# Optimization experiments

Hardware: AMD Instinct MI355X
Metric: run time of the kernel (lower is better)

Reference implementation:

```python
import jax, jax.numpy as jnp
import numpy as np

N_NODES = 100000
N_EDGES = 1600000
N_FEAT = 128
N_HID = 128
N_CLASS = 10
N_GRAPHS = 512
BN_EPS = 1e-5


def setup_inputs() -> dict:
    key = jax.random.key(0)
    ks = jax.random.split(key, 12)
    x = jax.random.normal(ks[0], (N_NODES, N_FEAT), dtype=jnp.float32)
    edge_index = jax.random.randint(ks[1], (2, N_EDGES), 0, N_NODES, dtype=jnp.int32)
    batch = jnp.sort(jax.random.randint(ks[2], (N_NODES,), 0, N_GRAPHS, dtype=jnp.int32))
    s1 = 1.0 / np.sqrt(N_FEAT)
    s2 = 1.0 / np.sqrt(N_HID)
    W1 = jax.random.uniform(ks[3], (N_FEAT, N_HID), jnp.float32, -s1, s1)
    b1 = jax.random.uniform(ks[4], (N_HID,), jnp.float32, -s1, s1)
    gamma = jnp.ones((N_HID,), jnp.float32)
    beta = jnp.zeros((N_HID,), jnp.float32)
    W2 = jax.random.uniform(ks[5], (N_HID, N_HID), jnp.float32, -s2, s2)
    b2 = jax.random.uniform(ks[6], (N_HID,), jnp.float32, -s2, s2)
    clsW = jax.random.uniform(ks[7], (N_HID, N_CLASS), jnp.float32, -s2, s2)
    clsb = jax.random.uniform(ks[8], (N_CLASS,), jnp.float32, -s2, s2)
    return {"x": x, "edge_index": edge_index, "batch": batch,
            "W1": W1, "b1": b1, "gamma": gamma, "beta": beta,
            "W2": W2, "b2": b2, "clsW": clsW, "clsb": clsb}


def _gcn_norm(edge_index, n_nodes):
    # add self-loops, compute symmetric normalization D^-1/2 A_hat D^-1/2
    loops = jnp.arange(n_nodes, dtype=edge_index.dtype)
    src = jnp.concatenate([edge_index[0], loops])
    dst = jnp.concatenate([edge_index[1], loops])
    deg = jax.ops.segment_sum(jnp.ones_like(dst, dtype=jnp.float32), dst,
                              num_segments=n_nodes)
    dinv = jnp.where(deg > 0, jax.lax.rsqrt(deg), 0.0)
    norm = dinv[src] * dinv[dst]  # [E + N]
    return src, dst, norm


def _gcn_conv(h, src, dst, norm, W, b, n_nodes):
    h = h @ W                                   # [N, nhid] dense GEMM
    msg = h[src] * norm[:, None]                # gather + scale  [E+N, nhid]
    out = jax.ops.segment_sum(msg, dst, num_segments=n_nodes)  # scatter-add
    return out + b


def reference(x, edge_index, batch, W1, b1, gamma, beta, W2, b2, clsW, clsb):
    n_nodes = x.shape[0]
    src, dst, norm = _gcn_norm(edge_index, n_nodes)
    # layer 1: GCNConv -> BatchNorm(eval, running stats 0/1) -> ReLU -> Dropout(eval=id)
    h = _gcn_conv(x, src, dst, norm, W1, b1, n_nodes)
    h = h * (gamma / jnp.sqrt(1.0 + BN_EPS)) + beta
    h = jax.nn.relu(h)
    # layer 2: GCNConv (output layer, no bn/act)
    h = _gcn_conv(h, src, dst, norm, W2, b2, n_nodes)
    # global mean pool over batch index
    sums = jax.ops.segment_sum(h, batch, num_segments=N_GRAPHS)          # [G, nhid]
    cnts = jax.ops.segment_sum(jnp.ones((n_nodes,), h.dtype), batch,
                               num_segments=N_GRAPHS)
    g = sums / jnp.maximum(cnts, 1.0)[:, None]
    out = jax.nn.log_softmax(g @ clsW + clsb, axis=1)                    # [G, nclass]
    return out, g
```

## Files before the change

kernel.cpp:

```cpp
#include <hip/hip_runtime.h>
#include <hip/hip_bf16.h>

#define N_NODES 100000
#define N_EDGES 1600000
#define N_FEAT 128
#define N_HID 128
#define N_CLASS 10
#define N_GRAPHS 512
#define BN_RSQRT 0.9999950000374997f

#define NRANGE 12500
#define NSUB 512
#define SCAP 640
#define HGROUP 32
#define BPB (NSUB / HGROUP)

#define XT_STRIDE 136
#define YW_STRIDE 36

typedef _Float16 half_t;
typedef __attribute__((ext_vector_type(2))) _Float16 half2v;
typedef __attribute__((ext_vector_type(4))) _Float16 half4v;
typedef __attribute__((ext_vector_type(8))) _Float16 half8v;
typedef __attribute__((ext_vector_type(4))) float floatx4;
typedef __attribute__((ext_vector_type(2))) float floatx2;

__global__ __launch_bounds__(256) void bucket_fused(
    const int* __restrict__ src, const int* __restrict__ dst,
    int* __restrict__ cnt, unsigned long long* __restrict__ bucketed,
    const float* __restrict__ W1, half_t* __restrict__ Wt1,
    const float* __restrict__ W2, half_t* __restrict__ Wt2,
    const int* __restrict__ batch, int* __restrict__ boffs,
    int chunkE, int E, int nnodes)
{
    __shared__ int wcnt[4][8];
    __shared__ int wbase[4][8];
    int blk = blockIdx.x;
    if (blk >= NSUB) {
        int k = blk - NSUB;
        if (k < 128) {
            int i = k * 256 + threadIdx.x;
            const float* W = (i < 16384) ? W1 : W2;
            half_t* Wt = (i < 16384) ? Wt1 : Wt2;
            int j = i & 16383;
            int c = j >> 7, kk = j & 127;
            Wt[(size_t)c * 128 + kk] = (half_t)W[(size_t)kk * 128 + c];
        } else {
            int i = (k - 128) * 256 + threadIdx.x;
            if (i < nnodes) {
                int b = batch[i];
                int prev = (i == 0) ? -1 : batch[i - 1];
                for (int g = prev + 1; g <= b; ++g) boffs[g] = i;
                if (i == nnodes - 1)
                    for (int g = b + 1; g <= N_GRAPHS; ++g) boffs[g] = nnodes;
            }
        }
        return;
    }
    int b = blk;
    int wave = threadIdx.x >> 6;
    int lane = threadIdx.x & 63;
    int e0 = b * chunkE;
    int e1 = e0 + chunkE < E ? e0 + chunkE : E;
    int iters = (chunkE + 255) / 256;

    int mycnt = 0;
    for (int it = 0; it < iters; ++it) {
        int e = e0 + it * 256 + threadIdx.x;
        bool valid = e < e1;
        int d = valid ? dst[e] : 0;
        int rr = (d * 8) / N_NODES;
#pragma unroll
        for (int r = 0; r < 8; ++r) {
            unsigned long long m = __ballot(valid && rr == r);
            if (lane == r) mycnt += __popcll(m);
        }
    }
    if (lane < 8) wcnt[wave][lane] = mycnt;
    __syncthreads();
    if (threadIdx.x < 8) {
        int r = threadIdx.x;
        int s = 0;
#pragma unroll
        for (int w = 0; w < 4; ++w) { wbase[w][r] = s; s += wcnt[w][r]; }
        cnt[r * NSUB + b] = s;
    }
    __syncthreads();

    int myoff = (lane < 8) ? wbase[wave][lane] : 0;
    for (int it = 0; it < iters; ++it) {
        int e = e0 + it * 256 + threadIdx.x;
        bool valid = e < e1;
        int s = valid ? src[e] : 0;
        int d = valid ? dst[e] : 0;
        int rr = (d * 8) / N_NODES;
        unsigned long long pk = ((unsigned long long)(unsigned)d << 32) | (unsigned)s;
#pragma unroll
        for (int r = 0; r < 8; ++r) {
            unsigned long long m = __ballot(valid && rr == r);
            int base_r = __shfl(myoff, r);
            if (valid && rr == r) {
                int pos = base_r + __popcll(m & ((1ull << lane) - 1));
                if (pos < SCAP)
                    bucketed[(size_t)(r * NSUB + b) * SCAP + pos] = pk;
            }
            if (lane == r) myoff += __popcll(m);
        }
    }
}

__global__ __launch_bounds__(256) void hist2(
    const unsigned long long* __restrict__ bucketed, const int* __restrict__ cnt,
    int* __restrict__ partial)
{
    __shared__ int h[NRANGE];
    int r = blockIdx.x & 7, g = blockIdx.x >> 3;
    for (int i = threadIdx.x; i < NRANGE; i += 256) h[i] = 0;
    __syncthreads();
    int rbase = r * NRANGE;
    for (int j = 0; j < BPB; ++j) {
        int b = g * BPB + j;
        int n = cnt[r * NSUB + b];
        if (n > SCAP) n = SCAP;
        const unsigned long long* seg = bucketed + (size_t)(r * NSUB + b) * SCAP;
        for (int i = threadIdx.x; i < n; i += 256)
            atomicAdd(&h[(int)(seg[i] >> 32) - rbase], 1);
    }
    __syncthreads();
    int* slice = partial + (size_t)(r * HGROUP + g) * NRANGE;
    for (int i = threadIdx.x; i < NRANGE; i += 256) slice[i] = h[i];
}

__global__ void deg_reduce(const int* __restrict__ partial, int* __restrict__ deg,
                           float* __restrict__ dinv, int* __restrict__ bsums, int n) {
    __shared__ int sm[256];
    int t = threadIdx.x;
    int i = blockIdx.x * 256 + t;
    int s = 0;
    if (i < n) {
        int rr = i / NRANGE;
        int dl = i - rr * NRANGE;
        const int* p = partial + (size_t)rr * HGROUP * NRANGE + dl;
#pragma unroll 8
        for (int g = 0; g < HGROUP; ++g) s += p[(size_t)g * NRANGE];
        deg[i] = s;
        dinv[i] = rsqrtf((float)s + 1.0f);
    }
    sm[t] = s;
    __syncthreads();
    for (int off = 128; off > 0; off >>= 1) {
        if (t < off) sm[t] += sm[t + off];
        __syncthreads();
    }
    if (t == 0) bsums[blockIdx.x] = sm[0];
}

__global__ void scan_small(int* __restrict__ bsums, int nb) {
    __shared__ int buf[1024];
    int t = threadIdx.x;
    int v = (t < nb) ? bsums[t] : 0;
    buf[t] = v;
    __syncthreads();
    for (int off = 1; off < 1024; off <<= 1) {
        int x = (t >= off) ? buf[t - off] : 0;
        __syncthreads();
        buf[t] += x;
        __syncthreads();
    }
    if (t < nb) bsums[t] = buf[t] - v;
}

__global__ __launch_bounds__(256) void scan_chunkoff(
    const int* __restrict__ in, const int* __restrict__ bsums,
    int* __restrict__ rowptr, int* __restrict__ partial, int n, int total)
{
    __shared__ int s[256];
    int t = threadIdx.x;
    int i = blockIdx.x * 256 + t;
    int v = (i < n) ? in[i] : 0;
    s[t] = v;
    __syncthreads();
    for (int off = 1; off < 256; off <<= 1) {
        int x = (t >= off) ? s[t - off] : 0;
        __syncthreads();
        s[t] += x;
        __syncthreads();
    }
    if (i == 0) rowptr[n] = total;
    if (i < n) {
        int excl = bsums[blockIdx.x] + s[t] - v;
        rowptr[i] = excl;
        int rr = i / NRANGE;
        int dl = i - rr * NRANGE;
        int* p = partial + (size_t)rr * HGROUP * NRANGE + dl;
        int vals[32];
#pragma unroll
        for (int g = 0; g < 32; ++g) vals[g] = p[(size_t)g * NRANGE];
        int running = excl;
#pragma unroll
        for (int g = 0; g < 32; ++g) {
            int tmp = vals[g];
            p[(size_t)g * NRANGE] = running;
            running += tmp;
        }
    }
}

__global__ __launch_bounds__(256) void fill2(
    const unsigned long long* __restrict__ bucketed, const int* __restrict__ cnt,
    const int* __restrict__ partial, int* __restrict__ col)
{
    __shared__ int off[NRANGE];
    int r = blockIdx.x & 7, g = blockIdx.x >> 3;
    const int* slice = partial + (size_t)(r * HGROUP + g) * NRANGE;
    for (int i = threadIdx.x; i < NRANGE; i += 256) off[i] = slice[i];
    __syncthreads();
    int rbase = r * NRANGE;
    for (int j = 0; j < BPB; ++j) {
        int b = g * BPB + j;
        int n = cnt[r * NSUB + b];
        if (n > SCAP) n = SCAP;
        const unsigned long long* seg = bucketed + (size_t)(r * NSUB + b) * SCAP;
        for (int i = threadIdx.x; i < n; i += 256) {
            unsigned long long pk = seg[i];
            int pos = atomicAdd(&off[(int)(pk >> 32) - rbase], 1);
            col[pos] = (int)((unsigned)(pk & 0xffffffffu) << 7);
        }
    }
}

__global__ __launch_bounds__(256, 2) void gemm1_mfma(
    const float* __restrict__ X, const half_t* __restrict__ Wt,
    const float* __restrict__ dinv, unsigned char* __restrict__ Y8,
    int nrows, int ntiles)
{
    __shared__ __align__(16) half_t wlds[128 * XT_STRIDE];
    __shared__ __align__(16) half_t xb[2][64 * XT_STRIDE];
    __shared__ __align__(16) int yw_all[4 * 16 * YW_STRIDE];
    int tid = threadIdx.x;
    {
        const half8v* wg = (const half8v*)Wt;
        half8v w[8];
#pragma unroll
        for (int j = 0; j < 8; ++j) w[j] = wg[j * 256 + tid];
#pragma unroll
        for (int j = 0; j < 8; ++j) {
            int idx = j * 256 + tid;
            *(half8v*)(wlds + (idx >> 4) * XT_STRIDE + ((idx & 15) << 3)) = w[j];
        }
    }
    int wave = tid >> 6;
    int lane = tid & 63;
    int n16  = lane & 15;
    int quad = lane >> 4;
    int* yw = yw_all + wave * (16 * YW_STRIDE);

    int t = blockIdx.x;
    if (t >= ntiles) return;
    int cur = 0;
    {
        const float4* xg = (const float4*)(X + (size_t)t * 64 * 128);
        int idxmax = (nrows - t * 64) * 32;
#pragma unroll
        for (int j = 0; j < 8; ++j) {
            int idx = j * 256 + tid;
            if (idx < idxmax) {
                float4 f = xg[idx];
                half4v h = {(half_t)f.x, (half_t)f.y, (half_t)f.z, (half_t)f.w};
                *(half4v*)(xb[0] + (idx >> 5) * XT_STRIDE + ((idx & 31) << 2)) = h;
            }
        }
    }
    __syncthreads();
    for (;;) {
        int tn = t + gridDim.x;
        bool pf = tn < ntiles;
        float4 f[8];
        if (pf) {
            const float4* xg = (const float4*)(X + (size_t)tn * 64 * 128);
            int idxmax = (nrows - tn * 64) * 32;
#pragma unroll
            for (int j = 0; j < 8; ++j) {
                int idx = j * 256 + tid;
                f[j] = (idx < idxmax) ? xg[idx] : float4{0.f, 0.f, 0.f, 0.f};
            }
        }
        int r0 = t * 64 + wave * 16;
        bool active = r0 < nrows;
        int packedv[8];
        if (active) {
            const half_t* xr = xb[cur] + (wave * 16 + n16) * XT_STRIDE;
            half8v a0 = *(const half8v*)(xr + 0 * 32 + quad * 8);
            half8v a1 = *(const half8v*)(xr + 1 * 32 + quad * 8);
            half8v a2 = *(const half8v*)(xr + 2 * 32 + quad * 8);
            half8v a3 = *(const half8v*)(xr + 3 * 32 + quad * 8);
            float dr = dinv[r0 + n16];
#pragma unroll
            for (int c = 0; c < 8; ++c) {
                const half_t* wl = wlds + (c * 16 + n16) * XT_STRIDE;
                floatx4 acc = {0.f, 0.f, 0.f, 0.f};
                acc = __builtin_amdgcn_mfma_f32_16x16x32_f16(*(const half8v*)(wl + 0 * 32 + quad * 8), a0, acc, 0, 0, 0);
                acc = __builtin_amdgcn_mfma_f32_16x16x32_f16(*(const half8v*)(wl + 1 * 32 + quad * 8), a1, acc, 0, 0, 0);
                acc = __builtin_amdgcn_mfma_f32_16x16x32_f16(*(const half8v*)(wl + 2 * 32 + quad * 8), a2, acc, 0, 0, 0);
                acc = __builtin_amdgcn_mfma_f32_16x16x32_f16(*(const half8v*)(wl + 3 * 32 + quad * 8), a3, acc, 0, 0, 0);
                int packed = __builtin_amdgcn_cvt_pk_fp8_f32(acc[0] * dr, acc[1] * dr, 0, false);
                packed = __builtin_amdgcn_cvt_pk_fp8_f32(acc[2] * dr, acc[3] * dr, packed, true);
                packedv[c] = packed;
            }
#pragma unroll
            for (int c = 0; c < 8; ++c)
                yw[n16 * YW_STRIDE + c * 4 + quad] = packedv[c];
#pragma unroll
            for (int u = 0; u < 2; ++u) {
                int4 v = *(const int4*)(yw + (u * 8 + (lane >> 3)) * YW_STRIDE + (lane & 7) * 4);
                *(int4*)(Y8 + (size_t)r0 * 128 + u * 1024 + lane * 16) = v;
            }
        }
        __syncthreads();
        if (!pf) break;
        {
            int idxmax = (nrows - tn * 64) * 32;
#pragma unroll
            for (int j = 0; j < 8; ++j) {
                int idx = j * 256 + tid;
                if (idx < idxmax) {
                    half4v h = {(half_t)f[j].x, (half_t)f[j].y, (half_t)f[j].z, (half_t)f[j].w};
                    *(half4v*)(xb[cur ^ 1] + (idx >> 5) * XT_STRIDE + ((idx & 31) << 2)) = h;
                }
            }
        }
        __syncthreads();
        cur ^= 1;
        t = tn;
    }
}

__global__ __launch_bounds__(256, 2) void gemm2_mfma(
    const half_t* __restrict__ X, const half_t* __restrict__ Wt,
    const float* __restrict__ dinv, unsigned char* __restrict__ Y8,
    int nrows, int ntiles)
{
    __shared__ __align__(16) half_t wlds[128 * XT_STRIDE];
    __shared__ __align__(16) half_t xb[2][64 * XT_STRIDE];
    __shared__ __align__(16) int yw_all[4 * 16 * YW_STRIDE];
    int tid = threadIdx.x;
    {
        const half8v* wg = (const half8v*)Wt;
        half8v w[8];
#pragma unroll
        for (int j = 0; j < 8; ++j) w[j] = wg[j * 256 + tid];
#pragma unroll
        for (int j = 0; j < 8; ++j) {
            int idx = j * 256 + tid;
            *(half8v*)(wlds + (idx >> 4) * XT_STRIDE + ((idx & 15) << 3)) = w[j];
        }
    }
    int wave = tid >> 6;
    int lane = tid & 63;
    int n16  = lane & 15;
    int quad = lane >> 4;
    int* yw = yw_all + wave * (16 * YW_STRIDE);

    int t = blockIdx.x;
    if (t >= ntiles) return;
    int cur = 0;
    {
        const half8v* xg = (const half8v*)(X + (size_t)t * 64 * 128);
        int idxmax = (nrows - t * 64) * 16;
#pragma unroll
        for (int j = 0; j < 4; ++j) {
            int idx = j * 256 + tid;
            if (idx < idxmax)
                *(half8v*)(xb[0] + (idx >> 4) * XT_STRIDE + ((idx & 15) << 3)) = xg[idx];
        }
    }
    __syncthreads();
    for (;;) {
        int tn = t + gridDim.x;
        bool pf = tn < ntiles;
        half8v v[4];
        if (pf) {
            const half8v* xg = (const half8v*)(X + (size_t)tn * 64 * 128);
            int idxmax = (nrows - tn * 64) * 16;
#pragma unroll
            for (int j = 0; j < 4; ++j) {
                int idx = j * 256 + tid;
                if (idx < idxmax) v[j] = xg[idx];
            }
        }
        int r0 = t * 64 + wave * 16;
        bool active = r0 < nrows;
        int packedv[8];
        if (active) {
            const half_t* xr = xb[cur] + (wave * 16 + n16) * XT_STRIDE;
            half8v a0 = *(const half8v*)(xr + 0 * 32 + quad * 8);
            half8v a1 = *(const half8v*)(xr + 1 * 32 + quad * 8);
            half8v a2 = *(const half8v*)(xr + 2 * 32 + quad * 8);
            half8v a3 = *(const half8v*)(xr + 3 * 32 + quad * 8);
            float dr = dinv[r0 + n16];
#pragma unroll
            for (int c = 0; c < 8; ++c) {
                const half_t* wl = wlds + (c * 16 + n16) * XT_STRIDE;
                floatx4 acc = {0.f, 0.f, 0.f, 0.f};
                acc = __builtin_amdgcn_mfma_f32_16x16x32_f16(*(const half8v*)(wl + 0 * 32 + quad * 8), a0, acc, 0, 0, 0);
                acc = __builtin_amdgcn_mfma_f32_16x16x32_f16(*(const half8v*)(wl + 1 * 32 + quad * 8), a1, acc, 0, 0, 0);
                acc = __builtin_amdgcn_mfma_f32_16x16x32_f16(*(const half8v*)(wl + 2 * 32 + quad * 8), a2, acc, 0, 0, 0);
                acc = __builtin_amdgcn_mfma_f32_16x16x32_f16(*(const half8v*)(wl + 3 * 32 + quad * 8), a3, acc, 0, 0, 0);
                int packed = __builtin_amdgcn_cvt_pk_fp8_f32(acc[0] * dr, acc[1] * dr, 0, false);
                packed = __builtin_amdgcn_cvt_pk_fp8_f32(acc[2] * dr, acc[3] * dr, packed, true);
                packedv[c] = packed;
            }
#pragma unroll
            for (int c = 0; c < 8; ++c)
                yw[n16 * YW_STRIDE + c * 4 + quad] = packedv[c];
#pragma unroll
            for (int u = 0; u < 2; ++u) {
                int4 o = *(const int4*)(yw + (u * 8 + (lane >> 3)) * YW_STRIDE + (lane & 7) * 4);
                *(int4*)(Y8 + (size_t)r0 * 128 + u * 1024 + lane * 16) = o;
            }
        }
        __syncthreads();
        if (!pf) break;
        {
            int idxmax = (nrows - tn * 64) * 16;
#pragma unroll
            for (int j = 0; j < 4; ++j) {
                int idx = j * 256 + tid;
                if (idx < idxmax)
                    *(half8v*)(xb[cur ^ 1] + (idx >> 4) * XT_STRIDE + ((idx & 15) << 3)) = v[j];
            }
        }
        __syncthreads();
        cur ^= 1;
        t = tn;
    }
}

__global__ __launch_bounds__(256, 4) void agg_fp8(
    const unsigned char* __restrict__ hs, half_t* __restrict__ out,
    const int* __restrict__ col, const int* __restrict__ rowptr,
    const float* __restrict__ bias,
    const float* __restrict__ gamma, const float* __restrict__ beta,
    int nnodes, int do_bn_relu)
{
    int wave = threadIdx.x >> 6;
    int lane = threadIdx.x & 63;
    int q = lane >> 4;
    int l16 = lane & 15;
    int nb4 = (blockIdx.x * 4 + wave) * 4;
    int i = nb4 + q;
    bool valid = i < nnodes;
    unsigned iq = valid ? (unsigned)i : (unsigned)nnodes;
    unsigned f8 = (unsigned)l16 << 3;
    unsigned ZOFF = (unsigned)nnodes << 7;

    int e0 = valid ? rowptr[i] : 0;
    int e1 = valid ? rowptr[i + 1] : 0;
    int deg = e1 - e0;
    int m = deg;
    m = max(m, __shfl_xor(m, 16));
    m = max(m, __shfl_xor(m, 32));
    int nchunk = (m + 15) >> 4;

    unsigned long long us = *(const unsigned long long*)(hs + ((iq << 7) | f8));

    floatx2 a0 = {0.f, 0.f}, a1 = {0.f, 0.f}, a2 = {0.f, 0.f}, a3 = {0.f, 0.f};
    for (int t = 0; t < nchunk; ++t) {
        int idx = e0 + t * 16 + l16;
        unsigned cv = (idx < e1) ? (unsigned)col[idx] : ZOFF;
#pragma unroll
        for (int half = 0; half < 2; ++half) {
            const int kk = half * 8;
            unsigned long long v0, v1, v2, v3, v4, v5, v6, v7;
#define AGG_ADDR(K)                                                            \
            ({ unsigned sA = (unsigned)__builtin_amdgcn_readlane((int)cv, kk + K);      \
               unsigned sB = (unsigned)__builtin_amdgcn_readlane((int)cv, kk + K + 16); \
               unsigned sC = (unsigned)__builtin_amdgcn_readlane((int)cv, kk + K + 32); \
               unsigned sD = (unsigned)__builtin_amdgcn_readlane((int)cv, kk + K + 48); \
               unsigned rAB = (q & 1) ? sB : sA;                               \
               unsigned rCD = (q & 1) ? sD : sC;                               \
               unsigned rr = (q & 2) ? rCD : rAB;                              \
               *(const unsigned long long*)(hs + (rr | f8)); })
            v0 = AGG_ADDR(0);
            v1 = AGG_ADDR(1);
            v2 = AGG_ADDR(2);
            v3 = AGG_ADDR(3);
            v4 = AGG_ADDR(4);
            v5 = AGG_ADDR(5);
            v6 = AGG_ADDR(6);
            v7 = AGG_ADDR(7);
#undef AGG_ADDR
#define AGG_ACC(V)                                                             \
            { unsigned lo = (unsigned)(V), hi = (unsigned)((V) >> 32);         \
              a0 += __builtin_amdgcn_cvt_pk_f32_fp8((int)lo, false);           \
              a1 += __builtin_amdgcn_cvt_pk_f32_fp8((int)lo, true);            \
              a2 += __builtin_amdgcn_cvt_pk_f32_fp8((int)hi, false);           \
              a3 += __builtin_amdgcn_cvt_pk_f32_fp8((int)hi, true); }
            AGG_ACC(v0) AGG_ACC(v1) AGG_ACC(v2) AGG_ACC(v3)
            AGG_ACC(v4) AGG_ACC(v5) AGG_ACC(v6) AGG_ACC(v7)
#undef AGG_ACC
        }
    }
    {
        unsigned lo = (unsigned)us, hi = (unsigned)(us >> 32);
        a0 += __builtin_amdgcn_cvt_pk_f32_fp8((int)lo, false);
        a1 += __builtin_amdgcn_cvt_pk_f32_fp8((int)lo, true);
        a2 += __builtin_amdgcn_cvt_pk_f32_fp8((int)hi, false);
        a3 += __builtin_amdgcn_cvt_pk_f32_fp8((int)hi, true);
    }

    if (!valid) return;
    float di = rsqrtf((float)deg + 1.0f);
    int fbase = l16 * 8;
    float4 bi0 = *(const float4*)(bias + fbase);
    float4 bi1 = *(const float4*)(bias + fbase + 4);
    float o0 = fmaf(di, a0.x, bi0.x);
    float o1 = fmaf(di, a0.y, bi0.y);
    float o2 = fmaf(di, a1.x, bi0.z);
    float o3 = fmaf(di, a1.y, bi0.w);
    float o4 = fmaf(di, a2.x, bi1.x);
    float o5 = fmaf(di, a2.y, bi1.y);
    float o6 = fmaf(di, a3.x, bi1.z);
    float o7 = fmaf(di, a3.y, bi1.w);
    if (do_bn_relu) {
        float4 ga0 = *(const float4*)(gamma + fbase);
        float4 ga1 = *(const float4*)(gamma + fbase + 4);
        float4 be0 = *(const float4*)(beta + fbase);
        float4 be1 = *(const float4*)(beta + fbase + 4);
        o0 = fmaf(o0, ga0.x * BN_RSQRT, be0.x);
        o1 = fmaf(o1, ga0.y * BN_RSQRT, be0.y);
        o2 = fmaf(o2, ga0.z * BN_RSQRT, be0.z);
        o3 = fmaf(o3, ga0.w * BN_RSQRT, be0.w);
        o4 = fmaf(o4, ga1.x * BN_RSQRT, be1.x);
        o5 = fmaf(o5, ga1.y * BN_RSQRT, be1.y);
        o6 = fmaf(o6, ga1.z * BN_RSQRT, be1.z);
        o7 = fmaf(o7, ga1.w * BN_RSQRT, be1.w);
        o0 = o0 > 0.f ? o0 : 0.f;
        o1 = o1 > 0.f ? o1 : 0.f;
        o2 = o2 > 0.f ? o2 : 0.f;
        o3 = o3 > 0.f ? o3 : 0.f;
        o4 = o4 > 0.f ? o4 : 0.f;
        o5 = o5 > 0.f ? o5 : 0.f;
        o6 = o6 > 0.f ? o6 : 0.f;
        o7 = o7 > 0.f ? o7 : 0.f;
    }
    half8v ov = {(half_t)o0, (half_t)o1, (half_t)o2, (half_t)o3,
                 (half_t)o4, (half_t)o5, (half_t)o6, (half_t)o7};
    *(half8v*)(out + (size_t)i * 128 + fbase) = ov;
}

__global__ __launch_bounds__(512) void pool_cls(
    const half_t* __restrict__ h, const int* __restrict__ boffs,
    const float* __restrict__ clsW, const float* __restrict__ clsb,
    float* __restrict__ gout, float* __restrict__ out)
{
    __shared__ float red[8][128];
    __shared__ float zbuf[16];
    int g = blockIdx.x;
    int w = threadIdx.x >> 6;
    int lane = threadIdx.x & 63;
    int n0 = boffs[g], n1 = boffs[g + 1];
    float ax = 0.f, ay = 0.f;
    for (int n = n0 + w; n < n1; n += 8) {
        half2v v = *(const half2v*)(h + (size_t)n * 128 + lane * 2);
        ax += (float)v.x;
        ay += (float)v.y;
    }
    red[w][lane * 2] = ax;
    red[w][lane * 2 + 1] = ay;
    __syncthreads();
    if (w == 0) {
        float sx = 0.f, sy = 0.f;
#pragma unroll
        for (int j = 0; j < 8; ++j) {
            sx += red[j][lane * 2];
            sy += red[j][lane * 2 + 1];
        }
        float cnt = (float)((n1 - n0) > 1 ? (n1 - n0) : 1);
        float g0 = sx / cnt, g1 = sy / cnt;
        gout[(size_t)g * 128 + lane * 2] = g0;
        gout[(size_t)g * 128 + lane * 2 + 1] = g1;
        red[0][lane * 2] = g0;
        red[0][lane * 2 + 1] = g1;
    }
    __syncthreads();
    if (threadIdx.x < N_CLASS) {
        int c = threadIdx.x;
        float z = clsb[c];
        for (int k = 0; k < N_HID; ++k)
            z = fmaf(red[0][k], clsW[k * N_CLASS + c], z);
        zbuf[c] = z;
    }
    __syncthreads();
    if (threadIdx.x == 0) {
        float m = zbuf[0];
#pragma unroll
        for (int c = 1; c < N_CLASS; ++c) m = fmaxf(m, zbuf[c]);
        float s = 0.f;
#pragma unroll
        for (int c = 0; c < N_CLASS; ++c) s += expf(zbuf[c] - m);
        float l = logf(s);
#pragma unroll
        for (int c = 0; c < N_CLASS; ++c)
            out[(size_t)g * N_CLASS + c] = zbuf[c] - m - l;
    }
}

extern "C" void kernel_launch(void* const* d_in, const int* in_sizes, int n_in,
                              void* d_out, int out_size, void* d_ws, size_t ws_size,
                              hipStream_t stream) {
    const float* x     = (const float*)d_in[0];
    const int*   ei    = (const int*)d_in[1];
    const int*   batch = (const int*)d_in[2];
    const float* W1    = (const float*)d_in[3];
    const float* b1    = (const float*)d_in[4];
    const float* gamma = (const float*)d_in[5];
    const float* beta  = (const float*)d_in[6];
    const float* W2    = (const float*)d_in[7];
    const float* b2    = (const float*)d_in[8];
    const float* clsW  = (const float*)d_in[9];
    const float* clsb  = (const float*)d_in[10];

    const int N = in_sizes[0] / N_FEAT;
    const int E = in_sizes[1] / 2;
    const int* src = ei;
    const int* dst = ei + E;

    unsigned char* BA8 = (unsigned char*)d_ws;
    half_t* BB = (half_t*)(BA8 + (size_t)(N + 1) * 128);
    half_t* Wt1 = BB + (size_t)N * 128;
    half_t* Wt2 = Wt1 + 16384;
    int*   col     = (int*)(Wt2 + 16384);
    int*   rowptr  = col + E;
    int*   deg     = rowptr + (N + 4);
    float* dinv    = (float*)(deg + N);
    int*   cnt     = (int*)(dinv + N);
    unsigned long long* bucketed =
        (unsigned long long*)(cnt + 8 * NSUB);
    int*   partial = (int*)(bucketed + (size_t)8 * NSUB * SCAP);
    int*   boffs   = partial + 8 * HGROUP * NRANGE;
    int*   bsums   = boffs + N_GRAPHS + 4;

    const int nb = (N + 255) / 256;
    const int chunkE = (E + NSUB - 1) / NSUB;
    const int ntiles = (N + 63) / 64;
    const int gemmGrid = 512;
    const int aggBlocks = (N + 15) / 16;

    hipMemsetAsync(BA8 + (size_t)N * 128, 0, 128, stream);

    bucket_fused<<<NSUB + 128 + nb, 256, 0, stream>>>(
        src, dst, cnt, bucketed, W1, Wt1, W2, Wt2, batch, boffs, chunkE, E, N);
    hist2<<<8 * HGROUP, 256, 0, stream>>>(bucketed, cnt, partial);
    deg_reduce<<<nb, 256, 0, stream>>>(partial, deg, dinv, bsums, N);
    scan_small<<<1, 1024, 0, stream>>>(bsums, nb);
    scan_chunkoff<<<nb, 256, 0, stream>>>(deg, bsums, rowptr, partial, N, E);
    gemm1_mfma<<<gemmGrid, 256, 0, stream>>>(x, Wt1, dinv, BA8, N, ntiles);
    fill2<<<256, 256, 0, stream>>>(bucketed, cnt, partial, col);
    agg_fp8<<<aggBlocks, 256, 0, stream>>>(BA8, BB, col, rowptr, b1, gamma, beta, N, 1);
    gemm2_mfma<<<gemmGrid, 256, 0, stream>>>(BB, Wt2, dinv, BA8, N, ntiles);
    agg_fp8<<<aggBlocks, 256, 0, stream>>>(BA8, BB, col, rowptr, b2, gamma, beta, N, 0);

    float* out = (float*)d_out;
    float* gsec = out + (size_t)N_GRAPHS * N_CLASS;
    pool_cls<<<N_GRAPHS, 512, 0, stream>>>(BB, boffs, clsW, clsb, gsec, out);
}
```

Before: 286.5 us.

## Fuse CSR fill and first GEMM into one launch, drop memset

Merges the fill2 CSR column-fill kernel and gemm1_mfma into a single launch. The first 256 blocks do the fill and the remaining 512 do the GEMM tiles, sharing one raw LDS buffer, so the two independent stages run concurrently and one launch gap is removed. The separate hipMemsetAsync that zeroes the sentinel row is replaced by an extra block in bucket_fused. The fill blocks now declare about 77KB of LDS, which may limit occupancy for that part of the grid.

```diff
diff --git a/kernel.cpp b/kernel.cpp
--- a/kernel.cpp
+++ b/kernel.cpp
@@ -17,6 +17,7 @@
 
 #define XT_STRIDE 136
 #define YW_STRIDE 36
+#define FG_LDS 78848
 
 typedef _Float16 half_t;
 typedef __attribute__((ext_vector_type(2))) _Float16 half2v;
@@ -31,6 +32,7 @@
     const float* __restrict__ W1, half_t* __restrict__ Wt1,
     const float* __restrict__ W2, half_t* __restrict__ Wt2,
     const int* __restrict__ batch, int* __restrict__ boffs,
+    int* __restrict__ sentinel,
     int chunkE, int E, int nnodes)
 {
     __shared__ int wcnt[4][8];
@@ -38,15 +40,17 @@
     int blk = blockIdx.x;
     if (blk >= NSUB) {
         int k = blk - NSUB;
-        if (k < 128) {
-            int i = k * 256 + threadIdx.x;
+        if (k == 0) {
+            if (threadIdx.x < 32) sentinel[threadIdx.x] = 0;
+        } else if (k <= 128) {
+            int i = (k - 1) * 256 + threadIdx.x;
             const float* W = (i < 16384) ? W1 : W2;
             half_t* Wt = (i < 16384) ? Wt1 : Wt2;
             int j = i & 16383;
             int c = j >> 7, kk = j & 127;
             Wt[(size_t)c * 128 + kk] = (half_t)W[(size_t)kk * 128 + c];
         } else {
-            int i = (k - 128) * 256 + threadIdx.x;
+            int i = (k - 129) * 256 + threadIdx.x;
             if (i < nnodes) {
                 int b = batch[i];
                 int prev = (i == 0) ? -1 : batch[i - 1];
@@ -206,38 +210,39 @@
     }
 }
 
-__global__ __launch_bounds__(256) void fill2(
+__global__ __launch_bounds__(256, 2) void fill2_gemm1p(
     const unsigned long long* __restrict__ bucketed, const int* __restrict__ cnt,
-    const int* __restrict__ partial, int* __restrict__ col)
-{
-    __shared__ int off[NRANGE];
-    int r = blockIdx.x & 7, g = blockIdx.x >> 3;
-    const int* slice = partial + (size_t)(r * HGROUP + g) * NRANGE;
-    for (int i = threadIdx.x; i < NRANGE; i += 256) off[i] = slice[i];
-    __syncthreads();
-    int rbase = r * NRANGE;
-    for (int j = 0; j < BPB; ++j) {
-        int b = g * BPB + j;
-        int n = cnt[r * NSUB + b];
-        if (n > SCAP) n = SCAP;
-        const unsigned long long* seg = bucketed + (size_t)(r * NSUB + b) * SCAP;
-        for (int i = threadIdx.x; i < n; i += 256) {
-            unsigned long long pk = seg[i];
-            int pos = atomicAdd(&off[(int)(pk >> 32) - rbase], 1);
-            col[pos] = (int)((unsigned)(pk & 0xffffffffu) << 7);
-        }
-    }
-}
-
-__global__ __launch_bounds__(256, 2) void gemm1_mfma(
+    const int* __restrict__ partial, int* __restrict__ col,
     const float* __restrict__ X, const half_t* __restrict__ Wt,
     const float* __restrict__ dinv, unsigned char* __restrict__ Y8,
     int nrows, int ntiles)
 {
-    __shared__ __align__(16) half_t wlds[128 * XT_STRIDE];
-    __shared__ __align__(16) half_t xb[2][64 * XT_STRIDE];
-    __shared__ __align__(16) int yw_all[4 * 16 * YW_STRIDE];
+    __shared__ __align__(16) unsigned char smem[FG_LDS];
     int tid = threadIdx.x;
+    if (blockIdx.x < 256) {
+        int* off = (int*)smem;
+        int r = blockIdx.x & 7, g = blockIdx.x >> 3;
+        const int* slice = partial + (size_t)(r * HGROUP + g) * NRANGE;
+        for (int i = tid; i < NRANGE; i += 256) off[i] = slice[i];
+        __syncthreads();
+        int rbase = r * NRANGE;
+        for (int j = 0; j < BPB; ++j) {
+            int b = g * BPB + j;
+            int n = cnt[r * NSUB + b];
+            if (n > SCAP) n = SCAP;
+            const unsigned long long* seg = bucketed + (size_t)(r * NSUB + b) * SCAP;
+            for (int i = tid; i < n; i += 256) {
+                unsigned long long pk = seg[i];
+                int pos = atomicAdd(&off[(int)(pk >> 32) - rbase], 1);
+                col[pos] = (int)((unsigned)(pk & 0xffffffffu) << 7);
+            }
+        }
+        return;
+    }
+    half_t* wlds = (half_t*)smem;
+    half_t* xb0  = (half_t*)(smem + 34816);
+    half_t* xb1  = (half_t*)(smem + 52224);
+    int* yw_all  = (int*)(smem + 69632);
     {
         const half8v* wg = (const half8v*)Wt;
         half8v w[8];
@@ -254,10 +259,12 @@
     int n16  = lane & 15;
     int quad = lane >> 4;
     int* yw = yw_all + wave * (16 * YW_STRIDE);
-
-    int t = blockIdx.x;
+    int stride = gridDim.x - 256;
+
+    int t = blockIdx.x - 256;
     if (t >= ntiles) return;
-    int cur = 0;
+    half_t* xbc = xb0;
+    half_t* xbn = xb1;
     {
         const float4* xg = (const float4*)(X + (size_t)t * 64 * 128);
         int idxmax = (nrows - t * 64) * 32;
@@ -267,13 +274,13 @@
             if (idx < idxmax) {
                 float4 f = xg[idx];
                 half4v h = {(half_t)f.x, (half_t)f.y, (half_t)f.z, (half_t)f.w};
-                *(half4v*)(xb[0] + (idx >> 5) * XT_STRIDE + ((idx & 31) << 2)) = h;
+                *(half4v*)(xbc + (idx >> 5) * XT_STRIDE + ((idx & 31) << 2)) = h;
             }
         }
     }
     __syncthreads();
     for (;;) {
-        int tn = t + gridDim.x;
+        int tn = t + stride;
         bool pf = tn < ntiles;
         float4 f[8];
         if (pf) {
@@ -289,7 +296,7 @@
         bool active = r0 < nrows;
         int packedv[8];
         if (active) {
-            const half_t* xr = xb[cur] + (wave * 16 + n16) * XT_STRIDE;
+            const half_t* xr = xbc + (wave * 16 + n16) * XT_STRIDE;
             half8v a0 = *(const half8v*)(xr + 0 * 32 + quad * 8);
             half8v a1 = *(const half8v*)(xr + 1 * 32 + quad * 8);
             half8v a2 = *(const half8v*)(xr + 2 * 32 + quad * 8);
@@ -325,12 +332,12 @@
                 int idx = j * 256 + tid;
                 if (idx < idxmax) {
                     half4v h = {(half_t)f[j].x, (half_t)f[j].y, (half_t)f[j].z, (half_t)f[j].w};
-                    *(half4v*)(xb[cur ^ 1] + (idx >> 5) * XT_STRIDE + ((idx & 31) << 2)) = h;
+                    *(half4v*)(xbn + (idx >> 5) * XT_STRIDE + ((idx & 31) << 2)) = h;
                 }
             }
         }
         __syncthreads();
-        cur ^= 1;
+        half_t* tmp = xbc; xbc = xbn; xbn = tmp;
         t = tn;
     }
 }
@@ -644,21 +651,19 @@
     const int nb = (N + 255) / 256;
     const int chunkE = (E + NSUB - 1) / NSUB;
     const int ntiles = (N + 63) / 64;
-    const int gemmGrid = 512;
     const int aggBlocks = (N + 15) / 16;
 
-    hipMemsetAsync(BA8 + (size_t)N * 128, 0, 128, stream);
-
-    bucket_fused<<<NSUB + 128 + nb, 256, 0, stream>>>(
-        src, dst, cnt, bucketed, W1, Wt1, W2, Wt2, batch, boffs, chunkE, E, N);
+    bucket_fused<<<NSUB + 129 + nb, 256, 0, stream>>>(
+        src, dst, cnt, bucketed, W1, Wt1, W2, Wt2, batch, boffs,
+        (int*)(BA8 + (size_t)N * 128), chunkE, E, N);
     hist2<<<8 * HGROUP, 256, 0, stream>>>(bucketed, cnt, partial);
     deg_reduce<<<nb, 256, 0, stream>>>(partial, deg, dinv, bsums, N);
     scan_small<<<1, 1024, 0, stream>>>(bsums, nb);
     scan_chunkoff<<<nb, 256, 0, stream>>>(deg, bsums, rowptr, partial, N, E);
-    gemm1_mfma<<<gemmGrid, 256, 0, stream>>>(x, Wt1, dinv, BA8, N, ntiles);
-    fill2<<<256, 256, 0, stream>>>(bucketed, cnt, partial, col);
+    fill2_gemm1p<<<256 + 512, 256, 0, stream>>>(
+        bucketed, cnt, partial, col, x, Wt1, dinv, BA8, N, ntiles);
     agg_fp8<<<aggBlocks, 256, 0, stream>>>(BA8, BB, col, rowptr, b1, gamma, beta, N, 1);
-    gemm2_mfma<<<gemmGrid, 256, 0, stream>>>(BB, Wt2, dinv, BA8, N, ntiles);
+    gemm2_mfma<<<512, 256, 0, stream>>>(BB, Wt2, dinv, BA8, N, ntiles);
     agg_fp8<<<aggBlocks, 256, 0, stream>>>(BA8, BB, col, rowptr, b2, gamma, beta, N, 0);
 
     float* out = (float*)d_out;
```

New measurement: 281.0 us. Within noise of the previous version (-1.9%).
